# Optimization experiments

Measured on AMD Instinct MI355X. Metric: run time of the kernel, lower is better.

Reference implementation:

```python
import jax, jax.numpy as jnp
import numpy as np

N, E, B = 20000, 60000, 512
F_IN, ED, H, C = 7, 3, 4, 256
HC = H * C  # 1024
D_MODEL = 1024
EPS_BN = 1e-5


def setup_inputs() -> dict:
    key = jax.random.key(0)
    ks = jax.random.split(key, 24)
    s = 0.05
    inp = {
        'x': jax.random.normal(ks[0], (N, F_IN), jnp.float32),
        'edge_index': jax.random.randint(ks[1], (2, E), 0, N, jnp.int32),
        'edge_attr': jax.random.normal(ks[2], (E, ED), jnp.float32),
        'batch': jnp.sort(jax.random.randint(ks[3], (N,), 0, B, jnp.int32)),
        'w0': jax.random.normal(ks[4], (F_IN, HC), jnp.float32) * s,
        'w_rest': jax.random.normal(ks[5], (3, HC, HC), jnp.float32) * s,
        'w_edge': jax.random.normal(ks[6], (4, ED, HC), jnp.float32) * s,
        'att_src': jax.random.normal(ks[7], (4, H, C), jnp.float32) * s,
        'att_dst': jax.random.normal(ks[8], (4, H, C), jnp.float32) * s,
        'att_edge': jax.random.normal(ks[9], (4, H, C), jnp.float32) * s,
        'bias012': jax.random.normal(ks[10], (3, HC), jnp.float32) * s,
        'bias3': jax.random.normal(ks[11], (C,), jnp.float32) * s,
        'bn_gamma': jnp.ones((3, HC), jnp.float32),
        'bn_beta': jnp.zeros((3, HC), jnp.float32),
        'bn_mean': jnp.zeros((3, HC), jnp.float32),
        'bn_var': jnp.ones((3, HC), jnp.float32),
        'gate_w': jax.random.normal(ks[12], (C, 1), jnp.float32) * s,
        'gate_b': jnp.zeros((1,), jnp.float32),
        'proj_w': jax.random.normal(ks[13], (C, D_MODEL), jnp.float32) * s,
        'proj_b': jnp.zeros((D_MODEL,), jnp.float32),
    }
    return inp


def _gat_layer(x, ei, ea, W, We, a_s, a_d, a_e, bias, concat):
    # PyG GATConv with edge_dim, add_self_loops=True (fill_value='mean'), eval mode (no dropout)
    n = x.shape[0]
    sl = jnp.arange(n, dtype=ei.dtype)
    ea_mean = ea.mean(axis=0)
    ei = jnp.concatenate([ei, jnp.stack([sl, sl])], axis=1)            # [2, E+N]
    ea = jnp.concatenate([ea, jnp.broadcast_to(ea_mean, (n, ea.shape[1]))], axis=0)
    h = (x @ W).reshape(n, H, C)                                       # [N,H,C]
    alpha_src = jnp.einsum('nhc,hc->nh', h, a_s)
    alpha_dst = jnp.einsum('nhc,hc->nh', h, a_d)
    eh = (ea @ We).reshape(-1, H, C)
    alpha_e = jnp.einsum('ehc,hc->eh', eh, a_e)
    src, dst = ei[0], ei[1]
    alpha = jax.nn.leaky_relu(alpha_src[src] + alpha_dst[dst] + alpha_e, 0.2)  # [E+N,H]
    amax = jax.ops.segment_max(alpha, dst, num_segments=n)
    alpha = jnp.exp(alpha - amax[dst])
    denom = jax.ops.segment_sum(alpha, dst, num_segments=n)
    alpha = alpha / (denom[dst] + 1e-16)
    msg = h[src] * alpha[:, :, None]                                   # [E+N,H,C]
    out = jax.ops.segment_sum(msg, dst, num_segments=n)                # [N,H,C]
    out = out.reshape(n, H * C) if concat else out.mean(axis=1)
    return out + bias


def reference(x, edge_index, edge_attr, batch, w0, w_rest, w_edge, att_src, att_dst,
              att_edge, bias012, bias3, bn_gamma, bn_beta, bn_mean, bn_var,
              gate_w, gate_b, proj_w, proj_b):
    h = x
    for i in range(4):
        W = w0 if i == 0 else w_rest[i - 1]
        concat = i < 3
        b = bias012[i] if concat else bias3
        h = _gat_layer(h, edge_index, edge_attr, W, w_edge[i],
                       att_src[i], att_dst[i], att_edge[i], b, concat)
        if i < 3:
            # BatchNorm1d in eval mode, then ReLU (dropout is identity in eval)
            h = (h - bn_mean[i]) * (bn_gamma[i] / jnp.sqrt(bn_var[i] + EPS_BN)) + bn_beta[i]
            h = jax.nn.relu(h)
    # AttentionalAggregation: segment softmax over gate scores, weighted sum per graph
    gate = h @ gate_w + gate_b                                         # [N,1]
    gmax = jax.ops.segment_max(gate, batch, num_segments=B)
    g = jnp.exp(gate - gmax[batch])
    gsum = jax.ops.segment_sum(g, batch, num_segments=B)
    w = g / (gsum[batch] + 1e-16)
    graph = jax.ops.segment_sum(w * h, batch, num_segments=B)          # [B,256]
    return graph @ proj_w + proj_b                                     # [B,1024]
```

## Files before the change

kernel.cpp:

```cpp
#include <hip/hip_runtime.h>
#include <math.h>

#define NN 20000
#define NP 20480
#define EE 60000
#define BB 512
#define HC 1024
#define HH 4
#define CC 256

typedef _Float16 f16;
typedef f16 half8 __attribute__((ext_vector_type(8)));
typedef f16 f16x4 __attribute__((ext_vector_type(4)));
typedef float floatx4 __attribute__((ext_vector_type(4)));
typedef float floatx16 __attribute__((ext_vector_type(16)));

__device__ __forceinline__ size_t af_off(int n, int c) {
    int mblk = n >> 7, rr = n & 127;
    int iter = c >> 5, kc = c & 31;
    int kh = kc >> 4, kg = (kc >> 3) & 1, e = kc & 7;
    return ((((size_t)(mblk * 32 + iter) * 2 + kh) * 4 + (rr >> 5)) * 64 +
            (kg * 32 + (rr & 31))) * 8 + e;
}

__global__ void ea_sum_kernel(const float* __restrict__ ea, float* sums, int E_) {
    float s0 = 0.f, s1 = 0.f, s2 = 0.f;
    for (int e = blockIdx.x * 256 + threadIdx.x; e < E_; e += gridDim.x * 256) {
        s0 += ea[e * 3 + 0];
        s1 += ea[e * 3 + 1];
        s2 += ea[e * 3 + 2];
    }
    for (int o = 32; o; o >>= 1) {
        s0 += __shfl_down(s0, o);
        s1 += __shfl_down(s1, o);
        s2 += __shfl_down(s2, o);
    }
    if ((threadIdx.x & 63) == 0) {
        atomicAdd(&sums[0], s0);
        atomicAdd(&sums[1], s1);
        atomicAdd(&sums[2], s2);
    }
}

__global__ void hist_kernel(const int* __restrict__ ei, int* counts, int E_) {
    int e = blockIdx.x * 256 + threadIdx.x;
    if (e < E_) atomicAdd(&counts[ei[E_ + e]], 1);
}

__global__ void scan1_kernel(const int* __restrict__ counts, int* __restrict__ partial,
                             int* __restrict__ psums, int n) {
    __shared__ int sdata[256];
    int t = threadIdx.x;
    int i = blockIdx.x * 256 + t;
    int v = (i < n) ? counts[i] : 0;
    sdata[t] = v;
    __syncthreads();
#pragma unroll
    for (int off = 1; off < 256; off <<= 1) {
        int tmp = (t >= off) ? sdata[t - off] : 0;
        __syncthreads();
        sdata[t] += tmp;
        __syncthreads();
    }
    if (i < n) partial[i] = sdata[t];
    if (t == 255) psums[blockIdx.x] = sdata[255];
}

__global__ void scan2_kernel(int* __restrict__ psums, int nb) {
    __shared__ int sdata[128];
    int t = threadIdx.x;
    sdata[t] = (t < nb) ? psums[t] : 0;
    __syncthreads();
#pragma unroll
    for (int off = 1; off < 128; off <<= 1) {
        int tmp = (t >= off) ? sdata[t - off] : 0;
        __syncthreads();
        sdata[t] += tmp;
        __syncthreads();
    }
    if (t < nb) psums[t] = (t == 0) ? 0 : sdata[t - 1];
}

__global__ void scan3_kernel(const int* __restrict__ partial, const int* __restrict__ psums,
                             int* __restrict__ indptr, int n) {
    int i = blockIdx.x * 256 + threadIdx.x;
    if (i == 0) indptr[0] = 0;
    if (i < n) indptr[i + 1] = partial[i] + psums[blockIdx.x];
}

__global__ void scatter_kernel(const int* __restrict__ ei, const int* __restrict__ indptr,
                               int* fill, int* sorted, int* sdst, int E_) {
    int e = blockIdx.x * 256 + threadIdx.x;
    if (e >= E_) return;
    int d = ei[E_ + e];
    int pos = indptr[d] + atomicAdd(&fill[d], 1);
    sorted[pos] = e;
    sdst[pos] = d;
}

__global__ void bptr_kernel(const int* __restrict__ batch, int* bptr, int n, int nb) {
    int i = blockIdx.x * 256 + threadIdx.x;
    if (i >= n) return;
    int b = batch[i];
    if (i == 0) {
        for (int bb = 0; bb <= b; bb++) bptr[bb] = 0;
    } else {
        int pb = batch[i - 1];
        if (pb != b) {
            for (int bb = pb + 1; bb <= b; bb++) bptr[bb] = i;
        }
    }
    if (i == n - 1) {
        for (int bb = b + 1; bb <= nb; bb++) bptr[bb] = n;
    }
}

__global__ void wconv_kernel(const float* __restrict__ w_rest, f16* __restrict__ wt) {
    __shared__ float tile[64][65];
    int l = blockIdx.z;
    int bx = blockIdx.x * 64;
    int by = blockIdx.y * 64;
    int t = threadIdx.x;
    int tr = t >> 6, tc = t & 63;
#pragma unroll
    for (int i = 0; i < 16; i++) {
        int r = by + i * 4 + tr;
        tile[i * 4 + tr][tc] = w_rest[(size_t)l * 1048576 + (size_t)r * 1024 + bx + tc];
    }
    __syncthreads();
#pragma unroll
    for (int i = 0; i < 16; i++) {
        int n = bx + i * 4 + tr;
        wt[(size_t)l * 1048576 + (size_t)n * 1024 + by + tc] = (f16)tile[tc][i * 4 + tr];
    }
}

__global__ void bfrs_kernel(const f16* __restrict__ wt, f16* __restrict__ Bf) {
    int iter = blockIdx.x, nblk = blockIdx.y, l = blockIdx.z;
    const f16* wl = wt + (size_t)l * 1048576;
    f16* bl = Bf + (size_t)l * 1048576;
    int t = threadIdx.x;
    for (int c = t; c < 512; c += 256) {
        int kh = c >> 8, rem = c & 255, cg = rem >> 6, lane = rem & 63;
        int n = nblk * 128 + cg * 32 + (lane & 31);
        int k = iter * 32 + (kh * 2 + (lane >> 5)) * 8;
        half8 v = *(const half8*)&wl[(size_t)n * 1024 + k];
        *(half8*)&bl[(size_t)(nblk * 32 + iter) * 4096 + c * 8] = v;
    }
}

__global__ void mmat_all_kernel(const float* __restrict__ w_edge,
                                const float* __restrict__ att_edge,
                                const float* __restrict__ ea_sums, float* Mmat,
                                float* ae_self, float invE) {
    __shared__ float red[256];
    __shared__ float Ms[12];
    int l = blockIdx.x;
    int t = threadIdx.x;
    for (int dh = 0; dh < 12; dh++) {
        int d = dh >> 2, hh = dh & 3;
        float v = w_edge[l * 3072 + d * HC + hh * CC + t] * att_edge[l * HC + hh * CC + t];
        red[t] = v;
        __syncthreads();
        for (int o = 128; o; o >>= 1) {
            if (t < o) red[t] += red[t + o];
            __syncthreads();
        }
        if (t == 0) {
            Ms[dh] = red[0];
            Mmat[l * 12 + dh] = red[0];
        }
        __syncthreads();
    }
    if (t < 4) {
        float v = 0.f;
        for (int d = 0; d < 3; d++) v += ea_sums[d] * invE * Ms[d * 4 + t];
        ae_self[l * 4 + t] = v;
    }
}

__global__ void pack_kernel(const int* __restrict__ ei, const int* __restrict__ sorted,
                            const float* __restrict__ ea, const float* __restrict__ Mmat,
                            int* __restrict__ ssrc, float* __restrict__ aeh_pk) {
    int idx = blockIdx.x * 256 + threadIdx.x;
    if (idx >= EE) return;
    int eid = sorted[idx];
    ssrc[idx] = ei[eid];
    float a0 = ea[eid * 3 + 0], a1 = ea[eid * 3 + 1], a2 = ea[eid * 3 + 2];
#pragma unroll
    for (int l = 0; l < 4; l++) {
#pragma unroll
        for (int h = 0; h < 4; h++) {
            aeh_pk[(size_t)idx * 16 + l * 4 + h] =
                a0 * Mmat[l * 12 + h] + a1 * Mmat[l * 12 + 4 + h] + a2 * Mmat[l * 12 + 8 + h];
        }
    }
}

__global__ void edgep_kernel(const int* __restrict__ ssrc, const int* __restrict__ sdst,
                             const float* __restrict__ aeh_pk, const float* __restrict__ asrc,
                             const float* __restrict__ adst, float* __restrict__ pe,
                             int layer) {
    int i = blockIdx.x * 256 + threadIdx.x;
    if (i >= EE) return;
    int src = ssrc[i];
    int dst = sdst[i];
    float4 a = *(const float4*)&asrc[(size_t)src * 4];
    float4 d = *(const float4*)&adst[(size_t)dst * 4];
    float4 m = *(const float4*)&aeh_pk[(size_t)i * 16 + layer * 4];
    float r[4] = {a.x + d.x + m.x, a.y + d.y + m.y, a.z + d.z + m.z, a.w + d.w + m.w};
    float4 o;
#pragma unroll
    for (int k = 0; k < 4; k++) {
        float v = (r[k] > 0.f) ? r[k] : 0.2f * r[k];
        (&o.x)[k] = __expf(v);
    }
    *(float4*)&pe[(size_t)i * 4] = o;
}

__global__ void bnss_kernel(const float* __restrict__ bias012, const float* __restrict__ bn_g,
                            const float* __restrict__ bn_b, const float* __restrict__ bn_m,
                            const float* __restrict__ bn_v, float2* __restrict__ bnss) {
    int i = blockIdx.x * 256 + threadIdx.x;
    if (i >= 3 * HC) return;
    float s = bn_g[i] * rsqrtf(bn_v[i] + 1e-5f);
    float2 o;
    o.x = s;
    o.y = (bias012[i] - bn_m[i]) * s + bn_b[i];
    bnss[i] = o;
}

__global__ void wvec_kernel(const float* __restrict__ w_rest, const float* __restrict__ att_src,
                            const float* __restrict__ att_dst, float* __restrict__ wsv,
                            float* __restrict__ wdv) {
    int l = blockIdx.y;
    int k = blockIdx.x;
    int t = threadIdx.x;
    int hp = t >> 6, lane = t & 63;
    int col = hp * 256 + lane * 4;
    const float* wrow = w_rest + (size_t)l * 1048576 + (size_t)k * 1024;
    float4 w4 = *(const float4*)&wrow[col];
    float4 a4 = *(const float4*)&att_src[(l + 1) * HC + col];
    float4 d4 = *(const float4*)&att_dst[(l + 1) * HC + col];
    float sp = w4.x * a4.x + w4.y * a4.y + w4.z * a4.z + w4.w * a4.w;
    float dp = w4.x * d4.x + w4.y * d4.y + w4.z * d4.z + w4.w * d4.w;
    for (int m = 1; m < 64; m <<= 1) {
        sp += __shfl_xor(sp, m);
        dp += __shfl_xor(dp, m);
// ... 48 lines not shown
}

__global__ void agg0x_kernel(const float* __restrict__ x, const float* __restrict__ asrc,
                             const float* __restrict__ adst, const float* __restrict__ ae_self,
                             const int* __restrict__ ssrc, const float* __restrict__ pe,
                             const int* __restrict__ indptr, float* __restrict__ xagg) {
    int n = blockIdx.x * 256 + threadIdx.x;
    if (n >= NN) return;
    float4 as4 = *(const float4*)&asrc[(size_t)n * 4];
    float4 ad4 = *(const float4*)&adst[(size_t)n * 4];
    float adl[4] = {ad4.x, ad4.y, ad4.z, ad4.w};
    float asl[4] = {as4.x, as4.y, as4.z, as4.w};
    float xr[7];
#pragma unroll
    for (int f = 0; f < 7; f++) xr[f] = x[n * 7 + f];
    float denom[4];
    float xa[4][7];
#pragma unroll
    for (int h = 0; h < 4; h++) {
        float r = asl[h] + adl[h] + ae_self[h];
        r = (r > 0.f) ? r : 0.2f * r;
        float p = __expf(r);
        denom[h] = p;
#pragma unroll
        for (int f = 0; f < 7; f++) xa[h][f] = p * xr[f];
    }
    int s = indptr[n], e = indptr[n + 1];
    for (int idx = s; idx < e; idx++) {
        int src = ssrc[idx];
        float4 pv = *(const float4*)&pe[(size_t)idx * 4];
        float pl[4] = {pv.x, pv.y, pv.z, pv.w};
        float xs[7];
#pragma unroll
        for (int f = 0; f < 7; f++) xs[f] = x[src * 7 + f];
#pragma unroll
        for (int h = 0; h < 4; h++) {
            denom[h] += pl[h];
#pragma unroll
            for (int f = 0; f < 7; f++) xa[h][f] += pl[h] * xs[f];
        }
    }
#pragma unroll
    for (int h = 0; h < 4; h++) {
        float inv = 1.0f / (denom[h] + 1e-16f);
#pragma unroll
        for (int f = 0; f < 7; f++) xagg[(size_t)n * 28 + h * 7 + f] = xa[h][f] * inv;
    }
}

__global__ void gemm7f_kernel(const float* __restrict__ xagg, const float* __restrict__ w0,
                              const float2* __restrict__ bnss, const float* __restrict__ wsv,
                              const float* __restrict__ wdv, f16* __restrict__ outAf,
                              float* __restrict__ asrc_n, float* __restrict__ adst_n) {
    __shared__ float xs[28];
    __shared__ float red[32];
    int n = blockIdx.x, t = threadIdx.x;
    if (t < 28) xs[t] = xagg[(size_t)n * 28 + t];
    __syncthreads();
    int head = t >> 6;
    int j0 = t * 4;
    float sp[4] = {0.f, 0.f, 0.f, 0.f}, dp[4] = {0.f, 0.f, 0.f, 0.f};
    f16x4 o;
#pragma unroll
    for (int k = 0; k < 4; k++) {
        int j = j0 + k;
        float dot = 0.f;
#pragma unroll
        for (int f = 0; f < 7; f++) dot += xs[head * 7 + f] * w0[f * HC + j];
        float2 ss = bnss[j];
        float val = fmaxf(fmaf(dot, ss.x, ss.y), 0.f);
        o[k] = (f16)val;
        float4 w4s = *(const float4*)&wsv[(size_t)j * 4];
        float4 w4d = *(const float4*)&wdv[(size_t)j * 4];
        sp[0] += val * w4s.x; sp[1] += val * w4s.y;
        sp[2] += val * w4s.z; sp[3] += val * w4s.w;
        dp[0] += val * w4d.x; dp[1] += val * w4d.y;
        dp[2] += val * w4d.z; dp[3] += val * w4d.w;
    }
    *(f16x4*)&outAf[af_off(n, j0)] = o;
    int wave = t >> 6, lane = t & 63;
#pragma unroll
    for (int m = 1; m < 64; m <<= 1) {
#pragma unroll
        for (int j = 0; j < 4; j++) {
            sp[j] += __shfl_xor(sp[j], m);
            dp[j] += __shfl_xor(dp[j], m);
        }
    }
    if (lane == 0) {
#pragma unroll
        for (int j = 0; j < 4; j++) {
            red[wave * 8 + j] = sp[j];
            red[wave * 8 + 4 + j] = dp[j];
        }
    }
    __syncthreads();
    if (t < 8) {
        float v = red[t] + red[8 + t] + red[16 + t] + red[24 + t];
        if (t < 4) asrc_n[n * 4 + t] = v;
        else adst_n[n * 4 + (t - 4)] = v;
    }
}

__global__ __launch_bounds__(256) void mfma_gemm_kernel(const f16* __restrict__ Af,
                                                        const f16* __restrict__ Bf,
                                                        f16* __restrict__ C16) {
    int t = threadIdx.x;
    int wave = t >> 6, lane = t & 63;
    int gid = blockIdx.x;
    int g = gid >> 6, rblk = gid & 63;
    int nblk = rblk >> 3;
    int mblk = g * 8 + (rblk & 7);
    int rg0 = (wave >> 1) * 2;
    int cg0 = (wave & 1) * 2;

    floatx16 acc[2][2];
#pragma unroll
    for (int i = 0; i < 2; i++)
#pragma unroll
        for (int j = 0; j < 2; j++) acc[i][j] = (floatx16)(0.f);

    const f16* pa = Af + (size_t)mblk * 131072 + (size_t)lane * 8;
    const f16* pb = Bf + (size_t)nblk * 131072 + (size_t)lane * 8;

#pragma unroll 2
    for (int iter = 0; iter < 32; iter++) {
        size_t base = (size_t)iter * 4096;
        half8 afr[2][2], bfr[2][2];
#pragma unroll
        for (int kh = 0; kh < 2; kh++) {
#pragma unroll
            for (int i = 0; i < 2; i++) {
                afr[kh][i] = *(const half8*)&pa[base + kh * 2048 + (rg0 + i) * 512];
                bfr[kh][i] = *(const half8*)&pb[base + kh * 2048 + (cg0 + i) * 512];
            }
        }
#pragma unroll
        for (int kh = 0; kh < 2; kh++)
#pragma unroll
            for (int i = 0; i < 2; i++)
#pragma unroll
                for (int j = 0; j < 2; j++)
                    acc[i][j] = __builtin_amdgcn_mfma_f32_32x32x16_f16(bfr[kh][j], afr[kh][i],
                                                                       acc[i][j], 0, 0, 0);
    }

    int fr32 = lane & 31, kg = lane >> 5;
#pragma unroll
    for (int i = 0; i < 2; i++) {
        int row = mblk * 128 + rg0 * 32 + i * 32 + fr32;
#pragma unroll
        for (int j = 0; j < 2; j++) {
#pragma unroll
            for (int gq = 0; gq < 4; gq++) {
                f16x4 o;
#pragma unroll
                for (int r = 0; r < 4; r++) o[r] = (f16)acc[i][j][gq * 4 + r];
                *(f16x4*)&C16[(size_t)row * HC + nblk * 128 + cg0 * 32 + j * 32 + gq * 8 +
                              kg * 4] = o;
            }
        }
    }
}

__global__ void agg_kernel(const f16* __restrict__ h16, const float* __restrict__ asrc,
                           const float* __restrict__ adst, const float* __restrict__ ae_self,
                           const int* __restrict__ ssrc, const float* __restrict__ pe,
                           const int* __restrict__ indptr, const float2* __restrict__ bnss,
                           const float* __restrict__ wsv, const float* __restrict__ wdv,
                           const float* __restrict__ bias3, const float* __restrict__ gw,
                           const float* __restrict__ gb, f16* __restrict__ out16,
                           float* __restrict__ asrc_n, float* __restrict__ adst_n,
                           float* __restrict__ out3, float* __restrict__ gate,
                           int layer, int concat) {
    __shared__ float buf[1024];
    __shared__ float red[32];
    int n = blockIdx.x, t = threadIdx.x;
    int h = t >> 6, lane = t & 63;
    int c4 = t * 4;

    float r = asrc[n * 4 + h] + adst[n * 4 + h] + ae_self[layer * 4 + h];
    r = (r > 0.f) ? r : 0.2f * r;
    float p = __expf(r);
    float denom = p;
    float ax, ay, az, aw;
    {
        f16x4 v = *(const f16x4*)&h16[(size_t)n * HC + c4];
        ax = p * (float)v[0]; ay = p * (float)v[1];
        az = p * (float)v[2]; aw = p * (float)v[3];
    }
    int s = indptr[n], epos = indptr[n + 1];
    for (int base = s; base < epos; base += 4) {
        int rem = epos - base;
        int src[4];
        float pv[4];
#pragma unroll
        for (int j = 0; j < 4; j++) {
            if (j < rem) {
                src[j] = ssrc[base + j];
                pv[j] = pe[(size_t)(base + j) * 4 + h];
            } else {
                src[j] = n;
                pv[j] = 0.f;
            }
        }
        f16x4 u[4];
#pragma unroll
        for (int j = 0; j < 4; j++) u[j] = *(const f16x4*)&h16[(size_t)src[j] * HC + c4];
#pragma unroll
        for (int j = 0; j < 4; j++) {
            denom += pv[j];
            ax += pv[j] * (float)u[j][0];
            ay += pv[j] * (float)u[j][1];
            az += pv[j] * (float)u[j][2];
            aw += pv[j] * (float)u[j][3];
        }
    }
    float inv = 1.0f / (denom + 1e-16f);
    ax *= inv; ay *= inv; az *= inv; aw *= inv;

    if (concat) {
        float vals[4] = {ax, ay, az, aw};
        f16x4 o;
        float sp[4] = {0.f, 0.f, 0.f, 0.f}, dp[4] = {0.f, 0.f, 0.f, 0.f};
#pragma unroll
        for (int k = 0; k < 4; k++) {
            int j = c4 + k;
            float2 ss = bnss[j];
            float val = fmaxf(fmaf(vals[k], ss.x, ss.y), 0.f);
            o[k] = (f16)val;
            float4 w4s = *(const float4*)&wsv[(size_t)j * 4];
            float4 w4d = *(const float4*)&wdv[(size_t)j * 4];
            sp[0] += val * w4s.x; sp[1] += val * w4s.y;
            sp[2] += val * w4s.z; sp[3] += val * w4s.w;
            dp[0] += val * w4d.x; dp[1] += val * w4d.y;
            dp[2] += val * w4d.z; dp[3] += val * w4d.w;
        }
        *(f16x4*)&out16[af_off(n, c4)] = o;
#pragma unroll
        for (int m = 1; m < 64; m <<= 1) {
#pragma unroll
            for (int j = 0; j < 4; j++) {
                sp[j] += __shfl_xor(sp[j], m);
                dp[j] += __shfl_xor(dp[j], m);
            }
        }
        if (lane == 0) {
#pragma unroll
            for (int j = 0; j < 4; j++) {
                red[h * 8 + j] = sp[j];
                red[h * 8 + 4 + j] = dp[j];
            }
        }
        __syncthreads();
        if (t < 8) {
            float v = red[t] + red[8 + t] + red[16 + t] + red[24 + t];
            if (t < 4) asrc_n[n * 4 + t] = v;
            else adst_n[n * 4 + (t - 4)] = v;
        }
    } else {
        buf[c4 + 0] = ax;
        buf[c4 + 1] = ay;
        buf[c4 + 2] = az;
        buf[c4 + 3] = aw;
        __syncthreads();
        if (t < 64) {
            float gpart = 0.f;
#pragma unroll
            for (int k = 0; k < 4; k++) {
                int c = t * 4 + k;
                float v2 = 0.25f * (buf[c] + buf[256 + c] + buf[512 + c] + buf[768 + c]) +
                           bias3[c];
                out3[(size_t)n * CC + c] = v2;
                gpart += v2 * gw[c];
            }
            for (int o = 32; o; o >>= 1) gpart += __shfl_down(gpart, o);
            if (t == 0) gate[n] = gpart + gb[0];
        }
    }
}

__global__ void graphagg_kernel(const float* __restrict__ gate, const float* __restrict__ h3,
                                const int* __restrict__ bptr, float* __restrict__ graph) {
    __shared__ float red[256];
    __shared__ float wn[256];
    int b = blockIdx.x, t = threadIdx.x;
    int s = bptr[b], epos = bptr[b + 1];
    float m = -3.4e38f;
    for (int n = s + t; n < epos; n += 256) m = fmaxf(m, gate[n]);
    red[t] = m;
    __syncthreads();
    for (int o = 128; o; o >>= 1) {
        if (t < o) red[t] = fmaxf(red[t], red[t + o]);
        __syncthreads();
    }
    float mval = red[0];
    __syncthreads();
    float sum = 0.f;
    for (int n = s + t; n < epos; n += 256) sum += __expf(gate[n] - mval);
    red[t] = sum;
    __syncthreads();
    for (int o = 128; o; o >>= 1) {
        if (t < o) red[t] += red[t + o];
        __syncthreads();
    }
    float ssum = red[0];
    __syncthreads();
    float acc = 0.f;
    for (int base = s; base < epos; base += 256) {
        int n = base + t;
        wn[t] = (n < epos) ? __expf(gate[n] - mval) : 0.f;
        __syncthreads();
        int cnt = min(256, epos - base);
        for (int j = 0; j < cnt; j++) acc += wn[j] * h3[(size_t)(base + j) * CC + t];
        __syncthreads();
    }
    graph[b * CC + t] = acc / (ssum + 1e-16f);
}

__global__ void proj_kernel(const float* __restrict__ graph, const float* __restrict__ pw,
                            const float* __restrict__ pb, float* __restrict__ out) {
    __shared__ float g[256];
    int b = blockIdx.x, t = threadIdx.x;
    g[t] = graph[b * CC + t];
    __syncthreads();
    for (int j = t; j < 1024; j += 256) {
        float acc = pb[j];
        for (int c = 0; c < 256; c++) acc += g[c] * pw[c * 1024 + j];
        out[(size_t)b * 1024 + j] = acc;
    }
}

extern "C" void kernel_launch(void* const* d_in, const int* in_sizes, int n_in,
                              void* d_out, int out_size, void* d_ws, size_t ws_size,
                              hipStream_t stream) {
    const float* x = (const float*)d_in[0];
    const int* ei = (const int*)d_in[1];
    const float* ea = (const float*)d_in[2];
    const int* batch = (const int*)d_in[3];
    const float* w0 = (const float*)d_in[4];
    const float* w_rest = (const float*)d_in[5];
    const float* w_edge = (const float*)d_in[6];
    const float* att_src = (const float*)d_in[7];
    const float* att_dst = (const float*)d_in[8];
    const float* att_edge = (const float*)d_in[9];
    const float* bias012 = (const float*)d_in[10];
    const float* bias3 = (const float*)d_in[11];
    const float* bn_g = (const float*)d_in[12];
    const float* bn_b = (const float*)d_in[13];
    const float* bn_m = (const float*)d_in[14];
    const float* bn_v = (const float*)d_in[15];
    const float* gate_w = (const float*)d_in[16];
    const float* gate_b = (const float*)d_in[17];
    const float* proj_w = (const float*)d_in[18];
    const float* proj_b = (const float*)d_in[19];
    float* out = (float*)d_out;

    float* ws = (float*)d_ws;
    size_t off = 0;
    f16* h_lin = (f16*)(ws + off); off += (size_t)NP * HC / 2;
    f16* h_af = (f16*)(ws + off); off += (size_t)NP * HC / 2;
    float* h3 = ws + off; off += (size_t)NN * CC;
    f16* wt = (f16*)(ws + off); off += (size_t)3 * HC * HC / 2;
    f16* Bf = (f16*)(ws + off); off += (size_t)3 * HC * HC / 2;
    float* asrcA = ws + off; off += (size_t)NN * 4;
    float* adstA = ws + off; off += (size_t)NN * 4;
    float* asrcB = ws + off; off += (size_t)NN * 4;
    float* adstB = ws + off; off += (size_t)NN * 4;
    float* wsv = ws + off; off += (size_t)3 * HC * 4;
    float* wdv = ws + off; off += (size_t)3 * HC * 4;
    float* w0s = ws + off; off += 28;
    float* w0d = ws + off; off += 28;
    float2* bnss = (float2*)(ws + off); off += (size_t)3 * HC * 2;
    float* aeh_pk = ws + off; off += (size_t)EE * 16;
    float* pbuf = ws + off; off += (size_t)EE * 4;
    float* xagg = ws + off; off += (size_t)NN * 28;
    float* gate = ws + off; off += (size_t)NN;
    float* graph = ws + off; off += (size_t)BB * CC;
    float* ea_sums = ws + off; off += 4;
    float* Mmat = ws + off; off += 48;
    float* ae_self = ws + off; off += 16;
    int* counts = (int*)(ws + off); off += NN;
    int* partial = (int*)(ws + off); off += NN;
    int* psums = (int*)(ws + off); off += 128;
    int* indptr = (int*)(ws + off); off += NN + 1;
    int* fill = (int*)(ws + off); off += NN;
    int* sorted = (int*)(ws + off); off += EE;
    int* ssrc = (int*)(ws + off); off += EE;
    int* sdst = (int*)(ws + off); off += EE;
    int* bptr = (int*)(ws + off); off += BB + 1;

    hipMemsetAsync(ea_sums, 0, 4 * sizeof(float), stream);
    hipMemsetAsync(counts, 0, NN * sizeof(int), stream);
    hipMemsetAsync(fill, 0, NN * sizeof(int), stream);

    ea_sum_kernel<<<64, 256, 0, stream>>>(ea, ea_sums, EE);
    hist_kernel<<<(EE + 255) / 256, 256, 0, stream>>>(ei, counts, EE);
    int nblk = (NN + 255) / 256;
    scan1_kernel<<<nblk, 256, 0, stream>>>(counts, partial, psums, NN);
    scan2_kernel<<<1, 128, 0, stream>>>(psums, nblk);
    scan3_kernel<<<nblk, 256, 0, stream>>>(partial, psums, indptr, NN);
    scatter_kernel<<<(EE + 255) / 256, 256, 0, stream>>>(ei, indptr, fill, sorted, sdst, EE);
    bptr_kernel<<<(NN + 255) / 256, 256, 0, stream>>>(batch, bptr, NN, BB);
    wconv_kernel<<<dim3(16, 16, 3), 256, 0, stream>>>(w_rest, wt);
    bfrs_kernel<<<dim3(32, 8, 3), 256, 0, stream>>>(wt, Bf);
    mmat_all_kernel<<<4, 256, 0, stream>>>(w_edge, att_edge, ea_sums, Mmat, ae_self,
                                           1.0f / EE);
    pack_kernel<<<(EE + 255) / 256, 256, 0, stream>>>(ei, sorted, ea, Mmat, ssrc, aeh_pk);
    bnss_kernel<<<(3 * HC + 255) / 256, 256, 0, stream>>>(bias012, bn_g, bn_b, bn_m, bn_v,
                                                          bnss);
    wvec_kernel<<<dim3(1024, 3), 256, 0, stream>>>(w_rest, att_src, att_dst, wsv, wdv);
    w0vec_kernel<<<7, 256, 0, stream>>>(w0, att_src, att_dst, w0s, w0d);
    alpha0_kernel<<<(NN + 255) / 256, 256, 0, stream>>>(x, w0s, w0d, asrcA, adstA);

    edgep_kernel<<<(EE + 255) / 256, 256, 0, stream>>>(ssrc, sdst, aeh_pk, asrcA, adstA,
                                                       pbuf, 0);
    agg0x_kernel<<<(NN + 255) / 256, 256, 0, stream>>>(x, asrcA, adstA, ae_self, ssrc,
                                                       pbuf, indptr, xagg);
    gemm7f_kernel<<<NN, 256, 0, stream>>>(xagg, w0, bnss, wsv, wdv, h_af, asrcB, adstB);

    float* asrc_cur = asrcB;
    float* adst_cur = adstB;
    float* asrc_nxt = asrcA;
    float* adst_nxt = adstA;
    for (int i = 1; i < 4; i++) {
        mfma_gemm_kernel<<<(NP / 128) * (HC / 128), 256, 0, stream>>>(
            h_af, Bf + (size_t)(i - 1) * HC * HC, h_lin);
        edgep_kernel<<<(EE + 255) / 256, 256, 0, stream>>>(ssrc, sdst, aeh_pk, asrc_cur,
                                                           adst_cur, pbuf, i);
        agg_kernel<<<NN, 256, 0, stream>>>(
            h_lin, asrc_cur, adst_cur, ae_self, ssrc, pbuf, indptr, bnss + (size_t)i * HC,
            wsv + (size_t)i * HC * 4, wdv + (size_t)i * HC * 4, bias3, gate_w, gate_b,
            h_af, asrc_nxt, adst_nxt, h3, gate, i, (i < 3) ? 1 : 0);
        float* tmp = asrc_cur; asrc_cur = asrc_nxt; asrc_nxt = tmp;
        tmp = adst_cur; adst_cur = adst_nxt; adst_nxt = tmp;
    }

    graphagg_kernel<<<BB, 256, 0, stream>>>(gate, h3, bptr, graph);
    proj_kernel<<<BB, 256, 0, stream>>>(graph, proj_w, proj_b, out);
}
```

Before: 664.4 us.

## Fuse preprocessing kernels and process two nodes per block with wider vectors

Result: slower. 814.1 us (+22.5%).

```diff
diff --git a/kernel.cpp b/kernel.cpp
--- a/kernel.cpp
+++ b/kernel.cpp
@@ -12,7 +12,6 @@
 typedef _Float16 f16;
 typedef f16 half8 __attribute__((ext_vector_type(8)));
 typedef f16 f16x4 __attribute__((ext_vector_type(4)));
-typedef float floatx4 __attribute__((ext_vector_type(4)));
 typedef float floatx16 __attribute__((ext_vector_type(16)));
 
 __device__ __forceinline__ size_t af_off(int n, int c) {
@@ -23,12 +22,15 @@
             (kg * 32 + (rr & 31))) * 8 + e;
 }
 
-__global__ void ea_sum_kernel(const float* __restrict__ ea, float* sums, int E_) {
+__global__ void ea_hist_kernel(const float* __restrict__ ea, const int* __restrict__ ei,
+                               float* sums, int* counts, int E_) {
+    int e = blockIdx.x * 256 + threadIdx.x;
     float s0 = 0.f, s1 = 0.f, s2 = 0.f;
-    for (int e = blockIdx.x * 256 + threadIdx.x; e < E_; e += gridDim.x * 256) {
-        s0 += ea[e * 3 + 0];
-        s1 += ea[e * 3 + 1];
-        s2 += ea[e * 3 + 2];
+    if (e < E_) {
+        s0 = ea[e * 3 + 0];
+        s1 = ea[e * 3 + 1];
+        s2 = ea[e * 3 + 2];
+        atomicAdd(&counts[ei[E_ + e]], 1);
     }
     for (int o = 32; o; o >>= 1) {
         s0 += __shfl_down(s0, o);
@@ -40,11 +42,6 @@
         atomicAdd(&sums[1], s1);
         atomicAdd(&sums[2], s2);
     }
-}
-
-__global__ void hist_kernel(const int* __restrict__ ei, int* counts, int E_) {
-    int e = blockIdx.x * 256 + threadIdx.x;
-    if (e < E_) atomicAdd(&counts[ei[E_ + e]], 1);
 }
 
 __global__ void scan1_kernel(const int* __restrict__ counts, int* __restrict__ partial,
@@ -88,14 +85,25 @@
     if (i < n) indptr[i + 1] = partial[i] + psums[blockIdx.x];
 }
 
-__global__ void scatter_kernel(const int* __restrict__ ei, const int* __restrict__ indptr,
-                               int* fill, int* sorted, int* sdst, int E_) {
+__global__ void scatter_kernel(const int* __restrict__ ei, const float* __restrict__ ea,
+                               const float* __restrict__ Mmat, const int* __restrict__ indptr,
+                               int* fill, int* __restrict__ ssrc, int* __restrict__ sdst,
+                               float* __restrict__ aeh_pk, int E_) {
     int e = blockIdx.x * 256 + threadIdx.x;
     if (e >= E_) return;
     int d = ei[E_ + e];
     int pos = indptr[d] + atomicAdd(&fill[d], 1);
-    sorted[pos] = e;
+    ssrc[pos] = ei[e];
     sdst[pos] = d;
+    float a0 = ea[e * 3 + 0], a1 = ea[e * 3 + 1], a2 = ea[e * 3 + 2];
+#pragma unroll
+    for (int l = 0; l < 4; l++) {
+#pragma unroll
+        for (int h = 0; h < 4; h++) {
+            aeh_pk[(size_t)pos * 16 + l * 4 + h] =
+                a0 * Mmat[l * 12 + h] + a1 * Mmat[l * 12 + 4 + h] + a2 * Mmat[l * 12 + 8 + h];
+        }
+    }
 }
 
 __global__ void bptr_kernel(const int* __restrict__ batch, int* bptr, int n, int nb) {
@@ -115,7 +123,7 @@
     }
 }
 
-__global__ void wconv_kernel(const float* __restrict__ w_rest, f16* __restrict__ wt) {
+__global__ void wbf_kernel(const float* __restrict__ w_rest, f16* __restrict__ Bf) {
     __shared__ float tile[64][65];
     int l = blockIdx.z;
     int bx = blockIdx.x * 64;
@@ -124,28 +132,23 @@
     int tr = t >> 6, tc = t & 63;
 #pragma unroll
     for (int i = 0; i < 16; i++) {
-        int r = by + i * 4 + tr;
-        tile[i * 4 + tr][tc] = w_rest[(size_t)l * 1048576 + (size_t)r * 1024 + bx + tc];
-    }
-    __syncthreads();
-#pragma unroll
-    for (int i = 0; i < 16; i++) {
-        int n = bx + i * 4 + tr;
-        wt[(size_t)l * 1048576 + (size_t)n * 1024 + by + tc] = (f16)tile[tc][i * 4 + tr];
-    }
-}
-
-__global__ void bfrs_kernel(const f16* __restrict__ wt, f16* __restrict__ Bf) {
-    int iter = blockIdx.x, nblk = blockIdx.y, l = blockIdx.z;
-    const f16* wl = wt + (size_t)l * 1048576;
-    f16* bl = Bf + (size_t)l * 1048576;
-    int t = threadIdx.x;
-    for (int c = t; c < 512; c += 256) {
-        int kh = c >> 8, rem = c & 255, cg = rem >> 6, lane = rem & 63;
-        int n = nblk * 128 + cg * 32 + (lane & 31);
-        int k = iter * 32 + (kh * 2 + (lane >> 5)) * 8;
-        half8 v = *(const half8*)&wl[(size_t)n * 1024 + k];
-        *(half8*)&bl[(size_t)(nblk * 32 + iter) * 4096 + c * 8] = v;
+        int k = by + i * 4 + tr;
+        tile[i * 4 + tr][tc] = w_rest[(size_t)l * 1048576 + (size_t)k * 1024 + bx + tc];
+    }
+    __syncthreads();
+#pragma unroll
+    for (int i = 0; i < 2; i++) {
+        int ck = (t >> 6) * 2 + i;
+        int cn = t & 63;
+        int n = bx + cn, k0 = by + ck * 8;
+        f16 o[8];
+#pragma unroll
+        for (int e = 0; e < 8; e++) o[e] = (f16)tile[ck * 8 + e][cn];
+        int nblk = n >> 7, iter = k0 >> 5, kc = k0 & 31;
+        int kh = kc >> 4, kg = (kc >> 3) & 1, cg = (n >> 5) & 3, lr = n & 31;
+        size_t off = ((((size_t)(nblk * 32 + iter) * 2 + kh) * 4 + cg) * 64 +
+                      kg * 32 + lr) * 8;
+        *(half8*)&Bf[(size_t)l * 1048576 + off] = *(half8*)o;
     }
 }
 
@@ -176,24 +179,6 @@
         float v = 0.f;
         for (int d = 0; d < 3; d++) v += ea_sums[d] * invE * Ms[d * 4 + t];
         ae_self[l * 4 + t] = v;
-    }
-}
-
-__global__ void pack_kernel(const int* __restrict__ ei, const int* __restrict__ sorted,
-                            const float* __restrict__ ea, const float* __restrict__ Mmat,
-                            int* __restrict__ ssrc, float* __restrict__ aeh_pk) {
-    int idx = blockIdx.x * 256 + threadIdx.x;
-    if (idx >= EE) return;
-    int eid = sorted[idx];
-    ssrc[idx] = ei[eid];
-    float a0 = ea[eid * 3 + 0], a1 = ea[eid * 3 + 1], a2 = ea[eid * 3 + 2];
-#pragma unroll
-    for (int l = 0; l < 4; l++) {
-#pragma unroll
-        for (int h = 0; h < 4; h++) {
-            aeh_pk[(size_t)idx * 16 + l * 4 + h] =
-                a0 * Mmat[l * 12 + h] + a1 * Mmat[l * 12 + 4 + h] + a2 * Mmat[l * 12 + 8 + h];
-        }
     }
 }
 
@@ -348,21 +333,23 @@
                               const float2* __restrict__ bnss, const float* __restrict__ wsv,
                               const float* __restrict__ wdv, f16* __restrict__ outAf,
                               float* __restrict__ asrc_n, float* __restrict__ adst_n) {
-    __shared__ float xs[28];
-    __shared__ float red[32];
-    int n = blockIdx.x, t = threadIdx.x;
-    if (t < 28) xs[t] = xagg[(size_t)n * 28 + t];
-    __syncthreads();
-    int head = t >> 6;
-    int j0 = t * 4;
+    __shared__ float xs[2][28];
+    __shared__ float red[4][8];
+    int t = threadIdx.x;
+    int sub = t >> 7, tt = t & 127;
+    int n = blockIdx.x * 2 + sub;
+    if (t < 56) xs[t / 28][t % 28] = xagg[(size_t)blockIdx.x * 56 + t];
+    __syncthreads();
+    int h = tt >> 5;
+    int col0 = h * 256 + (tt & 31) * 8;
     float sp[4] = {0.f, 0.f, 0.f, 0.f}, dp[4] = {0.f, 0.f, 0.f, 0.f};
-    f16x4 o;
-#pragma unroll
-    for (int k = 0; k < 4; k++) {
-        int j = j0 + k;
+    f16 o[8];
+#pragma unroll
+    for (int k = 0; k < 8; k++) {
+        int j = col0 + k;
         float dot = 0.f;
 #pragma unroll
-        for (int f = 0; f < 7; f++) dot += xs[head * 7 + f] * w0[f * HC + j];
+        for (int f = 0; f < 7; f++) dot += xs[sub][h * 7 + f] * w0[f * HC + j];
         float2 ss = bnss[j];
         float val = fmaxf(fmaf(dot, ss.x, ss.y), 0.f);
         o[k] = (f16)val;
@@ -373,7 +360,7 @@
         dp[0] += val * w4d.x; dp[1] += val * w4d.y;
         dp[2] += val * w4d.z; dp[3] += val * w4d.w;
     }
-    *(f16x4*)&outAf[af_off(n, j0)] = o;
+    *(half8*)&outAf[af_off(n, col0)] = *(half8*)o;
     int wave = t >> 6, lane = t & 63;
 #pragma unroll
     for (int m = 1; m < 64; m <<= 1) {
@@ -386,21 +373,23 @@
     if (lane == 0) {
 #pragma unroll
         for (int j = 0; j < 4; j++) {
-            red[wave * 8 + j] = sp[j];
-            red[wave * 8 + 4 + j] = dp[j];
-        }
-    }
-    __syncthreads();
-    if (t < 8) {
-        float v = red[t] + red[8 + t] + red[16 + t] + red[24 + t];
-        if (t < 4) asrc_n[n * 4 + t] = v;
-        else adst_n[n * 4 + (t - 4)] = v;
-    }
-}
-
-__global__ __launch_bounds__(256) void mfma_gemm_kernel(const f16* __restrict__ Af,
-                                                        const f16* __restrict__ Bf,
-                                                        f16* __restrict__ C16) {
+            red[wave][j] = sp[j];
+            red[wave][4 + j] = dp[j];
+        }
+    }
+    __syncthreads();
+    if (t < 16) {
+        int node = t >> 3, j = t & 7;
+        float v = red[2 * node][j] + red[2 * node + 1][j];
+        int nn = blockIdx.x * 2 + node;
+        if (j < 4) asrc_n[nn * 4 + j] = v;
+        else adst_n[nn * 4 + (j - 4)] = v;
+    }
+}
+
+__global__ __launch_bounds__(256, 5) void mfma_gemm_kernel(const f16* __restrict__ Af,
+                                                           const f16* __restrict__ Bf,
+                                                           f16* __restrict__ C16) {
     int t = threadIdx.x;
     int wave = t >> 6, lane = t & 63;
     int gid = blockIdx.x;
@@ -419,7 +408,7 @@
     const f16* pa = Af + (size_t)mblk * 131072 + (size_t)lane * 8;
     const f16* pb = Bf + (size_t)nblk * 131072 + (size_t)lane * 8;
 
-#pragma unroll 2
+#pragma unroll 4
     for (int iter = 0; iter < 32; iter++) {
         size_t base = (size_t)iter * 4096;
         half8 afr[2][2], bfr[2][2];
@@ -469,21 +458,23 @@
                            float* __restrict__ asrc_n, float* __restrict__ adst_n,
                            float* __restrict__ out3, float* __restrict__ gate,
                            int layer, int concat) {
-    __shared__ float buf[1024];
-    __shared__ float red[32];
-    int n = blockIdx.x, t = threadIdx.x;
-    int h = t >> 6, lane = t & 63;
-    int c4 = t * 4;
+    __shared__ float buf3[2][1024];
+    __shared__ float red[4][8];
+    int t = threadIdx.x;
+    int sub = t >> 7, tt = t & 127;
+    int n = blockIdx.x * 2 + sub;
+    int h = tt >> 5;
+    int col0 = h * 256 + (tt & 31) * 8;
 
     float r = asrc[n * 4 + h] + adst[n * 4 + h] + ae_self[layer * 4 + h];
     r = (r > 0.f) ? r : 0.2f * r;
     float p = __expf(r);
     float denom = p;
-    float ax, ay, az, aw;
+    float acc[8];
     {
-        f16x4 v = *(const f16x4*)&h16[(size_t)n * HC + c4];
-        ax = p * (float)v[0]; ay = p * (float)v[1];
-        az = p * (float)v[2]; aw = p * (float)v[3];
+        half8 v = *(const half8*)&h16[(size_t)n * HC + col0];
+#pragma unroll
+        for (int k = 0; k < 8; k++) acc[k] = p * (float)v[k];
     }
     int s = indptr[n], epos = indptr[n + 1];
     for (int base = s; base < epos; base += 4) {
@@ -500,30 +491,26 @@
                 pv[j] = 0.f;
             }
         }
-        f16x4 u[4];
-#pragma unroll
-        for (int j = 0; j < 4; j++) u[j] = *(const f16x4*)&h16[(size_t)src[j] * HC + c4];
+        half8 u[4];
+#pragma unroll
+        for (int j = 0; j < 4; j++) u[j] = *(const half8*)&h16[(size_t)src[j] * HC + col0];
 #pragma unroll
         for (int j = 0; j < 4; j++) {
             denom += pv[j];
-            ax += pv[j] * (float)u[j][0];
-            ay += pv[j] * (float)u[j][1];
-            az += pv[j] * (float)u[j][2];
-            aw += pv[j] * (float)u[j][3];
+#pragma unroll
+            for (int k = 0; k < 8; k++) acc[k] += pv[j] * (float)u[j][k];
         }
     }
     float inv = 1.0f / (denom + 1e-16f);
-    ax *= inv; ay *= inv; az *= inv; aw *= inv;
 
     if (concat) {
-        float vals[4] = {ax, ay, az, aw};
-        f16x4 o;
+        f16 o[8];
         float sp[4] = {0.f, 0.f, 0.f, 0.f}, dp[4] = {0.f, 0.f, 0.f, 0.f};
 #pragma unroll
-        for (int k = 0; k < 4; k++) {
-            int j = c4 + k;
+        for (int k = 0; k < 8; k++) {
+            int j = col0 + k;
             float2 ss = bnss[j];
-            float val = fmaxf(fmaf(vals[k], ss.x, ss.y), 0.f);
+            float val = fmaxf(fmaf(acc[k] * inv, ss.x, ss.y), 0.f);
             o[k] = (f16)val;
             float4 w4s = *(const float4*)&wsv[(size_t)j * 4];
             float4 w4d = *(const float4*)&wdv[(size_t)j * 4];
@@ -532,7 +519,8 @@
             dp[0] += val * w4d.x; dp[1] += val * w4d.y;
             dp[2] += val * w4d.z; dp[3] += val * w4d.w;
         }
-        *(f16x4*)&out16[af_off(n, c4)] = o;
+        *(half8*)&out16[af_off(n, col0)] = *(half8*)o;
+        int wave = t >> 6, lane = t & 63;
 #pragma unroll
         for (int m = 1; m < 64; m <<= 1) {
 #pragma unroll
@@ -544,34 +532,35 @@
         if (lane == 0) {
 #pragma unroll
             for (int j = 0; j < 4; j++) {
-                red[h * 8 + j] = sp[j];
-                red[h * 8 + 4 + j] = dp[j];
+                red[wave][j] = sp[j];
+                red[wave][4 + j] = dp[j];
             }
         }
         __syncthreads();
-        if (t < 8) {
-            float v = red[t] + red[8 + t] + red[16 + t] + red[24 + t];
-            if (t < 4) asrc_n[n * 4 + t] = v;
-            else adst_n[n * 4 + (t - 4)] = v;
+        if (t < 16) {
+            int node = t >> 3, j = t & 7;
+            float v = red[2 * node][j] + red[2 * node + 1][j];
+            int nn = blockIdx.x * 2 + node;
+            if (j < 4) asrc_n[nn * 4 + j] = v;
+            else adst_n[nn * 4 + (j - 4)] = v;
         }
     } else {
-        buf[c4 + 0] = ax;
-        buf[c4 + 1] = ay;
-        buf[c4 + 2] = az;
-        buf[c4 + 3] = aw;
-        __syncthreads();
-        if (t < 64) {
+#pragma unroll
+        for (int k = 0; k < 8; k++) buf3[sub][col0 + k] = acc[k] * inv;
+        __syncthreads();
+        if (h == 0) {
+            int cc0 = (tt & 31) * 8;
             float gpart = 0.f;
 #pragma unroll
-            for (int k = 0; k < 4; k++) {
-                int c = t * 4 + k;
-                float v2 = 0.25f * (buf[c] + buf[256 + c] + buf[512 + c] + buf[768 + c]) +
-                           bias3[c];
-                out3[(size_t)n * CC + c] = v2;
-                gpart += v2 * gw[c];
+            for (int k = 0; k < 8; k++) {
+                int cc = cc0 + k;
+                float v2 = 0.25f * (buf3[sub][cc] + buf3[sub][256 + cc] +
+                                    buf3[sub][512 + cc] + buf3[sub][768 + cc]) + bias3[cc];
+                out3[(size_t)n * CC + cc] = v2;
+                gpart += v2 * gw[cc];
             }
-            for (int o = 32; o; o >>= 1) gpart += __shfl_down(gpart, o);
-            if (t == 0) gate[n] = gpart + gb[0];
+            for (int o2 = 16; o2; o2 >>= 1) gpart += __shfl_down(gpart, o2);
+            if ((tt & 31) == 0) gate[n] = gpart + gb[0];
         }
     }
 }
@@ -616,14 +605,21 @@
 
 __global__ void proj_kernel(const float* __restrict__ graph, const float* __restrict__ pw,
                             const float* __restrict__ pb, float* __restrict__ out) {
-    __shared__ float g[256];
-    int b = blockIdx.x, t = threadIdx.x;
-    g[t] = graph[b * CC + t];
+    __shared__ float g[2][256];
+    int b0 = blockIdx.x * 2, t = threadIdx.x;
+    g[0][t] = graph[(size_t)b0 * CC + t];
+    g[1][t] = graph[(size_t)(b0 + 1) * CC + t];
     __syncthreads();
     for (int j = t; j < 1024; j += 256) {
-        float acc = pb[j];
-        for (int c = 0; c < 256; c++) acc += g[c] * pw[c * 1024 + j];
-        out[(size_t)b * 1024 + j] = acc;
+        float bj = pb[j];
+        float a0 = bj, a1 = bj;
+        for (int c = 0; c < 256; c++) {
+            float w = pw[c * 1024 + j];
+            a0 += g[0][c] * w;
+            a1 += g[1][c] * w;
+        }
+        out[(size_t)b0 * 1024 + j] = a0;
+        out[(size_t)(b0 + 1) * 1024 + j] = a1;
     }
 }
 
@@ -657,7 +653,6 @@
     f16* h_lin = (f16*)(ws + off); off += (size_t)NP * HC / 2;
     f16* h_af = (f16*)(ws + off); off += (size_t)NP * HC / 2;
     float* h3 = ws + off; off += (size_t)NN * CC;
-    f16* wt = (f16*)(ws + off); off += (size_t)3 * HC * HC / 2;
     f16* Bf = (f16*)(ws + off); off += (size_t)3 * HC * HC / 2;
     float* asrcA = ws + off; off += (size_t)NN * 4;
     float* adstA = ws + off; off += (size_t)NN * 4;
@@ -673,36 +668,31 @@
     float* xagg = ws + off; off += (size_t)NN * 28;
     float* gate = ws + off; off += (size_t)NN;
     float* graph = ws + off; off += (size_t)BB * CC;
-    float* ea_sums = ws + off; off += 4;
     float* Mmat = ws + off; off += 48;
     float* ae_self = ws + off; off += 16;
     int* counts = (int*)(ws + off); off += NN;
+    int* fill = (int*)(ws + off); off += NN;
+    float* ea_sums = ws + off; off += 4;
     int* partial = (int*)(ws + off); off += NN;
     int* psums = (int*)(ws + off); off += 128;
     int* indptr = (int*)(ws + off); off += NN + 1;
-    int* fill = (int*)(ws + off); off += NN;
-    int* sorted = (int*)(ws + off); off += EE;
     int* ssrc = (int*)(ws + off); off += EE;
     int* sdst = (int*)(ws + off); off += EE;
     int* bptr = (int*)(ws + off); off += BB + 1;
 
-    hipMemsetAsync(ea_sums, 0, 4 * sizeof(float), stream);
-    hipMemsetAsync(counts, 0, NN * sizeof(int), stream);
-    hipMemsetAsync(fill, 0, NN * sizeof(int), stream);
-
-    ea_sum_kernel<<<64, 256, 0, stream>>>(ea, ea_sums, EE);
-    hist_kernel<<<(EE + 255) / 256, 256, 0, stream>>>(ei, counts, EE);
+    hipMemsetAsync(counts, 0, (2 * NN + 4) * sizeof(int), stream);
+
+    ea_hist_kernel<<<(EE + 255) / 256, 256, 0, stream>>>(ea, ei, ea_sums, counts, EE);
     int nblk = (NN + 255) / 256;
     scan1_kernel<<<nblk, 256, 0, stream>>>(counts, partial, psums, NN);
     scan2_kernel<<<1, 128, 0, stream>>>(psums, nblk);
     scan3_kernel<<<nblk, 256, 0, stream>>>(partial, psums, indptr, NN);
-    scatter_kernel<<<(EE + 255) / 256, 256, 0, stream>>>(ei, indptr, fill, sorted, sdst, EE);
-    bptr_kernel<<<(NN + 255) / 256, 256, 0, stream>>>(batch, bptr, NN, BB);
-    wconv_kernel<<<dim3(16, 16, 3), 256, 0, stream>>>(w_rest, wt);
-    bfrs_kernel<<<dim3(32, 8, 3), 256, 0, stream>>>(wt, Bf);
     mmat_all_kernel<<<4, 256, 0, stream>>>(w_edge, att_edge, ea_sums, Mmat, ae_self,
                                            1.0f / EE);
-    pack_kernel<<<(EE + 255) / 256, 256, 0, stream>>>(ei, sorted, ea, Mmat, ssrc, aeh_pk);
+    scatter_kernel<<<(EE + 255) / 256, 256, 0, stream>>>(ei, ea, Mmat, indptr, fill, ssrc,
+                                                         sdst, aeh_pk, EE);
+    bptr_kernel<<<(NN + 255) / 256, 256, 0, stream>>>(batch, bptr, NN, BB);
+    wbf_kernel<<<dim3(16, 16, 3), 256, 0, stream>>>(w_rest, Bf);
     bnss_kernel<<<(3 * HC + 255) / 256, 256, 0, stream>>>(bias012, bn_g, bn_b, bn_m, bn_v,
                                                           bnss);
     wvec_kernel<<<dim3(1024, 3), 256, 0, stream>>>(w_rest, att_src, att_dst, wsv, wdv);
@@ -713,7 +703,7 @@
                                                        pbuf, 0);
     agg0x_kernel<<<(NN + 255) / 256, 256, 0, stream>>>(x, asrcA, adstA, ae_self, ssrc,
                                                        pbuf, indptr, xagg);
-    gemm7f_kernel<<<NN, 256, 0, stream>>>(xagg, w0, bnss, wsv, wdv, h_af, asrcB, adstB);
+    gemm7f_kernel<<<NN / 2, 256, 0, stream>>>(xagg, w0, bnss, wsv, wdv, h_af, asrcB, adstB);
 
     float* asrc_cur = asrcB;
     float* adst_cur = adstB;
@@ -724,7 +714,7 @@
             h_af, Bf + (size_t)(i - 1) * HC * HC, h_lin);
         edgep_kernel<<<(EE + 255) / 256, 256, 0, stream>>>(ssrc, sdst, aeh_pk, asrc_cur,
                                                            adst_cur, pbuf, i);
-        agg_kernel<<<NN, 256, 0, stream>>>(
+        agg_kernel<<<NN / 2, 256, 0, stream>>>(
             h_lin, asrc_cur, adst_cur, ae_self, ssrc, pbuf, indptr, bnss + (size_t)i * HC,
             wsv + (size_t)i * HC * 4, wdv + (size_t)i * HC * 4, bias3, gate_w, gate_b,
             h_af, asrc_nxt, adst_nxt, h3, gate, i, (i < 3) ? 1 : 0);
@@ -733,5 +723,5 @@
     }
 
     graphagg_kernel<<<BB, 256, 0, stream>>>(gate, h3, bptr, graph);
-    proj_kernel<<<BB, 256, 0, stream>>>(graph, proj_w, proj_b, out);
-}
+    proj_kernel<<<BB / 2, 256, 0, stream>>>(graph, proj_w, proj_b, out);
+}
```

## Fuse preprocessing kernels, merge weight conversion, tune GEMM unroll, batch projection rows

Applied to the files above, without the earlier changes.

Result: slower. 686.2 us (+3.3%).

```diff
diff --git a/kernel.cpp b/kernel.cpp
--- a/kernel.cpp
+++ b/kernel.cpp
@@ -12,7 +12,6 @@
 typedef _Float16 f16;
 typedef f16 half8 __attribute__((ext_vector_type(8)));
 typedef f16 f16x4 __attribute__((ext_vector_type(4)));
-typedef float floatx4 __attribute__((ext_vector_type(4)));
 typedef float floatx16 __attribute__((ext_vector_type(16)));
 
 __device__ __forceinline__ size_t af_off(int n, int c) {
@@ -23,12 +22,15 @@
             (kg * 32 + (rr & 31))) * 8 + e;
 }
 
-__global__ void ea_sum_kernel(const float* __restrict__ ea, float* sums, int E_) {
+__global__ void ea_hist_kernel(const float* __restrict__ ea, const int* __restrict__ ei,
+                               float* sums, int* counts, int E_) {
+    int e = blockIdx.x * 256 + threadIdx.x;
     float s0 = 0.f, s1 = 0.f, s2 = 0.f;
-    for (int e = blockIdx.x * 256 + threadIdx.x; e < E_; e += gridDim.x * 256) {
-        s0 += ea[e * 3 + 0];
-        s1 += ea[e * 3 + 1];
-        s2 += ea[e * 3 + 2];
+    if (e < E_) {
+        s0 = ea[e * 3 + 0];
+        s1 = ea[e * 3 + 1];
+        s2 = ea[e * 3 + 2];
+        atomicAdd(&counts[ei[E_ + e]], 1);
     }
     for (int o = 32; o; o >>= 1) {
         s0 += __shfl_down(s0, o);
@@ -40,11 +42,6 @@
         atomicAdd(&sums[1], s1);
         atomicAdd(&sums[2], s2);
     }
-}
-
-__global__ void hist_kernel(const int* __restrict__ ei, int* counts, int E_) {
-    int e = blockIdx.x * 256 + threadIdx.x;
-    if (e < E_) atomicAdd(&counts[ei[E_ + e]], 1);
 }
 
 __global__ void scan1_kernel(const int* __restrict__ counts, int* __restrict__ partial,
@@ -88,14 +85,25 @@
     if (i < n) indptr[i + 1] = partial[i] + psums[blockIdx.x];
 }
 
-__global__ void scatter_kernel(const int* __restrict__ ei, const int* __restrict__ indptr,
-                               int* fill, int* sorted, int* sdst, int E_) {
+__global__ void scatter_kernel(const int* __restrict__ ei, const float* __restrict__ ea,
+                               const float* __restrict__ Mmat, const int* __restrict__ indptr,
+                               int* fill, int* __restrict__ ssrc, int* __restrict__ sdst,
+                               float* __restrict__ aeh_pk, int E_) {
     int e = blockIdx.x * 256 + threadIdx.x;
     if (e >= E_) return;
     int d = ei[E_ + e];
     int pos = indptr[d] + atomicAdd(&fill[d], 1);
-    sorted[pos] = e;
+    ssrc[pos] = ei[e];
     sdst[pos] = d;
+    float a0 = ea[e * 3 + 0], a1 = ea[e * 3 + 1], a2 = ea[e * 3 + 2];
+#pragma unroll
+    for (int l = 0; l < 4; l++) {
+#pragma unroll
+        for (int h = 0; h < 4; h++) {
+            aeh_pk[(size_t)pos * 16 + l * 4 + h] =
+                a0 * Mmat[l * 12 + h] + a1 * Mmat[l * 12 + 4 + h] + a2 * Mmat[l * 12 + 8 + h];
+        }
+    }
 }
 
 __global__ void bptr_kernel(const int* __restrict__ batch, int* bptr, int n, int nb) {
@@ -115,7 +123,7 @@
     }
 }
 
-__global__ void wconv_kernel(const float* __restrict__ w_rest, f16* __restrict__ wt) {
+__global__ void wbf_kernel(const float* __restrict__ w_rest, f16* __restrict__ Bf) {
     __shared__ float tile[64][65];
     int l = blockIdx.z;
     int bx = blockIdx.x * 64;
@@ -124,28 +132,23 @@
     int tr = t >> 6, tc = t & 63;
 #pragma unroll
     for (int i = 0; i < 16; i++) {
-        int r = by + i * 4 + tr;
-        tile[i * 4 + tr][tc] = w_rest[(size_t)l * 1048576 + (size_t)r * 1024 + bx + tc];
-    }
-    __syncthreads();
-#pragma unroll
-    for (int i = 0; i < 16; i++) {
-        int n = bx + i * 4 + tr;
-        wt[(size_t)l * 1048576 + (size_t)n * 1024 + by + tc] = (f16)tile[tc][i * 4 + tr];
-    }
-}
-
-__global__ void bfrs_kernel(const f16* __restrict__ wt, f16* __restrict__ Bf) {
-    int iter = blockIdx.x, nblk = blockIdx.y, l = blockIdx.z;
-    const f16* wl = wt + (size_t)l * 1048576;
-    f16* bl = Bf + (size_t)l * 1048576;
-    int t = threadIdx.x;
-    for (int c = t; c < 512; c += 256) {
-        int kh = c >> 8, rem = c & 255, cg = rem >> 6, lane = rem & 63;
-        int n = nblk * 128 + cg * 32 + (lane & 31);
-        int k = iter * 32 + (kh * 2 + (lane >> 5)) * 8;
-        half8 v = *(const half8*)&wl[(size_t)n * 1024 + k];
-        *(half8*)&bl[(size_t)(nblk * 32 + iter) * 4096 + c * 8] = v;
+        int k = by + i * 4 + tr;
+        tile[i * 4 + tr][tc] = w_rest[(size_t)l * 1048576 + (size_t)k * 1024 + bx + tc];
+    }
+    __syncthreads();
+#pragma unroll
+    for (int i = 0; i < 2; i++) {
+        int ck = (t >> 6) * 2 + i;
+        int cn = t & 63;
+        int n = bx + cn, k0 = by + ck * 8;
+        f16 o[8];
+#pragma unroll
+        for (int e = 0; e < 8; e++) o[e] = (f16)tile[ck * 8 + e][cn];
+        int nblk = n >> 7, iter = k0 >> 5, kc = k0 & 31;
+        int kh = kc >> 4, kg = (kc >> 3) & 1, cg = (n >> 5) & 3, lr = n & 31;
+        size_t off = ((((size_t)(nblk * 32 + iter) * 2 + kh) * 4 + cg) * 64 +
+                      kg * 32 + lr) * 8;
+        *(half8*)&Bf[(size_t)l * 1048576 + off] = *(half8*)o;
     }
 }
 
@@ -176,24 +179,6 @@
         float v = 0.f;
         for (int d = 0; d < 3; d++) v += ea_sums[d] * invE * Ms[d * 4 + t];
         ae_self[l * 4 + t] = v;
-    }
-}
-
-__global__ void pack_kernel(const int* __restrict__ ei, const int* __restrict__ sorted,
-                            const float* __restrict__ ea, const float* __restrict__ Mmat,
-                            int* __restrict__ ssrc, float* __restrict__ aeh_pk) {
-    int idx = blockIdx.x * 256 + threadIdx.x;
-    if (idx >= EE) return;
-    int eid = sorted[idx];
-    ssrc[idx] = ei[eid];
-    float a0 = ea[eid * 3 + 0], a1 = ea[eid * 3 + 1], a2 = ea[eid * 3 + 2];
-#pragma unroll
-    for (int l = 0; l < 4; l++) {
-#pragma unroll
-        for (int h = 0; h < 4; h++) {
-            aeh_pk[(size_t)idx * 16 + l * 4 + h] =
-                a0 * Mmat[l * 12 + h] + a1 * Mmat[l * 12 + 4 + h] + a2 * Mmat[l * 12 + 8 + h];
-        }
     }
 }
 
@@ -398,9 +383,9 @@
     }
 }
 
-__global__ __launch_bounds__(256) void mfma_gemm_kernel(const f16* __restrict__ Af,
-                                                        const f16* __restrict__ Bf,
-                                                        f16* __restrict__ C16) {
+__global__ __launch_bounds__(256, 5) void mfma_gemm_kernel(const f16* __restrict__ Af,
+                                                           const f16* __restrict__ Bf,
+                                                           f16* __restrict__ C16) {
     int t = threadIdx.x;
     int wave = t >> 6, lane = t & 63;
     int gid = blockIdx.x;
@@ -419,7 +404,7 @@
     const f16* pa = Af + (size_t)mblk * 131072 + (size_t)lane * 8;
     const f16* pb = Bf + (size_t)nblk * 131072 + (size_t)lane * 8;
 
-#pragma unroll 2
+#pragma unroll 4
     for (int iter = 0; iter < 32; iter++) {
         size_t base = (size_t)iter * 4096;
         half8 afr[2][2], bfr[2][2];
@@ -616,14 +601,21 @@
 
 __global__ void proj_kernel(const float* __restrict__ graph, const float* __restrict__ pw,
                             const float* __restrict__ pb, float* __restrict__ out) {
-    __shared__ float g[256];
-    int b = blockIdx.x, t = threadIdx.x;
-    g[t] = graph[b * CC + t];
+    __shared__ float g[2][256];
+    int b0 = blockIdx.x * 2, t = threadIdx.x;
+    g[0][t] = graph[(size_t)b0 * CC + t];
+    g[1][t] = graph[(size_t)(b0 + 1) * CC + t];
     __syncthreads();
     for (int j = t; j < 1024; j += 256) {
-        float acc = pb[j];
-        for (int c = 0; c < 256; c++) acc += g[c] * pw[c * 1024 + j];
-        out[(size_t)b * 1024 + j] = acc;
+        float bj = pb[j];
+        float a0 = bj, a1 = bj;
+        for (int c = 0; c < 256; c++) {
+            float w = pw[c * 1024 + j];
+            a0 += g[0][c] * w;
+            a1 += g[1][c] * w;
+        }
+        out[(size_t)b0 * 1024 + j] = a0;
+        out[(size_t)(b0 + 1) * 1024 + j] = a1;
     }
 }
 
@@ -657,7 +649,6 @@
     f16* h_lin = (f16*)(ws + off); off += (size_t)NP * HC / 2;
     f16* h_af = (f16*)(ws + off); off += (size_t)NP * HC / 2;
     float* h3 = ws + off; off += (size_t)NN * CC;
-    f16* wt = (f16*)(ws + off); off += (size_t)3 * HC * HC / 2;
     f16* Bf = (f16*)(ws + off); off += (size_t)3 * HC * HC / 2;
     float* asrcA = ws + off; off += (size_t)NN * 4;
     float* adstA = ws + off; off += (size_t)NN * 4;
@@ -673,36 +664,31 @@
     float* xagg = ws + off; off += (size_t)NN * 28;
     float* gate = ws + off; off += (size_t)NN;
     float* graph = ws + off; off += (size_t)BB * CC;
-    float* ea_sums = ws + off; off += 4;
     float* Mmat = ws + off; off += 48;
     float* ae_self = ws + off; off += 16;
     int* counts = (int*)(ws + off); off += NN;
+    int* fill = (int*)(ws + off); off += NN;
+    float* ea_sums = ws + off; off += 4;
     int* partial = (int*)(ws + off); off += NN;
     int* psums = (int*)(ws + off); off += 128;
     int* indptr = (int*)(ws + off); off += NN + 1;
-    int* fill = (int*)(ws + off); off += NN;
-    int* sorted = (int*)(ws + off); off += EE;
     int* ssrc = (int*)(ws + off); off += EE;
     int* sdst = (int*)(ws + off); off += EE;
     int* bptr = (int*)(ws + off); off += BB + 1;
 
-    hipMemsetAsync(ea_sums, 0, 4 * sizeof(float), stream);
-    hipMemsetAsync(counts, 0, NN * sizeof(int), stream);
-    hipMemsetAsync(fill, 0, NN * sizeof(int), stream);
-
-    ea_sum_kernel<<<64, 256, 0, stream>>>(ea, ea_sums, EE);
-    hist_kernel<<<(EE + 255) / 256, 256, 0, stream>>>(ei, counts, EE);
+    hipMemsetAsync(counts, 0, (2 * NN + 4) * sizeof(int), stream);
+
+    ea_hist_kernel<<<(EE + 255) / 256, 256, 0, stream>>>(ea, ei, ea_sums, counts, EE);
     int nblk = (NN + 255) / 256;
     scan1_kernel<<<nblk, 256, 0, stream>>>(counts, partial, psums, NN);
     scan2_kernel<<<1, 128, 0, stream>>>(psums, nblk);
     scan3_kernel<<<nblk, 256, 0, stream>>>(partial, psums, indptr, NN);
-    scatter_kernel<<<(EE + 255) / 256, 256, 0, stream>>>(ei, indptr, fill, sorted, sdst, EE);
-    bptr_kernel<<<(NN + 255) / 256, 256, 0, stream>>>(batch, bptr, NN, BB);
-    wconv_kernel<<<dim3(16, 16, 3), 256, 0, stream>>>(w_rest, wt);
-    bfrs_kernel<<<dim3(32, 8, 3), 256, 0, stream>>>(wt, Bf);
     mmat_all_kernel<<<4, 256, 0, stream>>>(w_edge, att_edge, ea_sums, Mmat, ae_self,
                                            1.0f / EE);
-    pack_kernel<<<(EE + 255) / 256, 256, 0, stream>>>(ei, sorted, ea, Mmat, ssrc, aeh_pk);
+    scatter_kernel<<<(EE + 255) / 256, 256, 0, stream>>>(ei, ea, Mmat, indptr, fill, ssrc,
+                                                         sdst, aeh_pk, EE);
+    bptr_kernel<<<(NN + 255) / 256, 256, 0, stream>>>(batch, bptr, NN, BB);
+    wbf_kernel<<<dim3(16, 16, 3), 256, 0, stream>>>(w_rest, Bf);
     bnss_kernel<<<(3 * HC + 255) / 256, 256, 0, stream>>>(bias012, bn_g, bn_b, bn_m, bn_v,
                                                           bnss);
     wvec_kernel<<<dim3(1024, 3), 256, 0, stream>>>(w_rest, att_src, att_dst, wsv, wdv);
@@ -733,5 +719,5 @@
     }
 
     graphagg_kernel<<<BB, 256, 0, stream>>>(gate, h3, bptr, graph);
-    proj_kernel<<<BB, 256, 0, stream>>>(graph, proj_w, proj_b, out);
-}
+    proj_kernel<<<BB / 2, 256, 0, stream>>>(graph, proj_w, proj_b, out);
+}
```
